# Kernel optimization log

Hardware: AMD Instinct MI355X
Metric: run time of the kernel (lower is better)

Reference implementation:

```python
import jax, jax.numpy as jnp
import numpy as np

THRESHOLD = 0.1
EPS = 1e-05


def setup_inputs() -> dict:
    key = jax.random.key(0)
    kx, kl, k1, k2 = jax.random.split(key, 4)
    B, S, D = 8, 4096, 1024
    Dh = max(2, D // 2)
    x = jax.random.normal(kx, (B, S, D), dtype=jnp.float32)
    # trailing (right) padding with random valid lengths in [S//2, S]
    lengths = jax.random.randint(kl, (B,), S // 2, S + 1)
    pad = jnp.arange(S)[None, :] >= lengths[:, None]  # [B, S] bool, True = padded
    W1 = jax.random.normal(k1, (D, Dh), dtype=jnp.float32) * (1.0 / np.sqrt(D))
    b1 = jnp.zeros((Dh,), dtype=jnp.float32)
    W2 = jax.random.normal(k2, (Dh, 1), dtype=jnp.float32) * (1.0 / np.sqrt(Dh))
    b2 = jnp.zeros((1,), dtype=jnp.float32)
    return {"x": x, "pad": pad, "W1": W1, "b1": b1, "W2": W2, "b2": b2}


def reference(x, pad, W1, b1, W2, b2):
    B, S, D = x.shape
    pos = jnp.arange(S)
    # number of valid (non-pad) tokens per batch; pad is trailing
    length = S - jnp.sum(pad, axis=1)  # [B]

    # tiny gate MLP: Linear -> ReLU -> Linear, squashed to (0, 1)
    h = jax.nn.relu(jnp.einsum('bsd,dh->bsh', x, W1) + b1)
    y = jnp.einsum('bsh,ho->bso', h, W2) + b2          # [B, S, 1]
    y = (1.0 + jnp.tanh(10.0 * y)) * 0.5

    # zero out gate values at padded positions (torch loop: y[i, n:] = 0)
    valid = pos[None, :] < length[:, None]             # [B, S]
    y = jnp.where(valid[..., None], y, 0.0)

    # lift so at least one token passes the threshold
    adjust = jnp.clip(EPS + THRESHOLD - jnp.max(y, axis=1), 0.0)  # [B, 1]
    y = y + adjust[:, None, :]                         # broadcast over seq

    u = x * y                                          # gated features [B, S, D]
    ys = y[..., 0]                                     # [B, S]
    u_mask = (ys > THRESHOLD) & (~pad)                 # tokens kept
    new_len = jnp.sum(u_mask, axis=1)                  # [B]

    # compact kept tokens to the front of each row (stable sort: kept first,
    # original order preserved) -- the mask-scatter v[v_mask] = u[u_mask]
    order = jnp.argsort(~u_mask, axis=1, stable=True)  # [B, S]
    v = jnp.take_along_axis(u, order[..., None], axis=1)
    v_mask = pos[None, :] < new_len[:, None]           # [B, S]
    v = jnp.where(v_mask[..., None], v, 0.0)
    v_pad = ~v_mask
    return v, v_pad
```

## Files before the change

### kernel.cpp

```cpp
#include <hip/hip_runtime.h>
#include <math.h>

#define NB 8
#define NS 4096
#define ND 1024
#define NDH 512
#define NTOK (NB*NS)
#define THRESH 0.1f
#define EPSV 1e-5f

using short8   = __attribute__((ext_vector_type(8)))  short;
using floatx16 = __attribute__((ext_vector_type(16))) float;
using floatv4  = __attribute__((ext_vector_type(4)))  float;

__device__ __forceinline__ unsigned short f32_to_bf16_rne(float f) {
  union { float f; unsigned u; } v; v.f = f;
  unsigned r = v.u + 0x7fffu + ((v.u >> 16) & 1u);
  return (unsigned short)(r >> 16);
}
__device__ __forceinline__ float bf16_to_f32(unsigned short h) {
  union { unsigned u; float f; } v; v.u = ((unsigned)h) << 16;
  return v.f;
}

__device__ __forceinline__ void cvt8_split(const float4& a, const float4& b,
                                           short8& hi, short8& lo) {
  float v8[8] = {a.x, a.y, a.z, a.w, b.x, b.y, b.z, b.w};
  unsigned hp[4], lp[4];
#pragma unroll
  for (int j = 0; j < 4; ++j) {
    unsigned short h0 = f32_to_bf16_rne(v8[2 * j]);
    unsigned short h1 = f32_to_bf16_rne(v8[2 * j + 1]);
    unsigned short l0 = f32_to_bf16_rne(v8[2 * j] - bf16_to_f32(h0));
    unsigned short l1 = f32_to_bf16_rne(v8[2 * j + 1] - bf16_to_f32(h1));
    hp[j] = (unsigned)h0 | ((unsigned)h1 << 16);
    lp[j] = (unsigned)l0 | ((unsigned)l1 << 16);
  }
  *(uint4*)&hi = make_uint4(hp[0], hp[1], hp[2], hp[3]);
  *(uint4*)&lo = make_uint4(lp[0], lp[1], lp[2], lp[3]);
}

__global__ __launch_bounds__(256)
void k0_prep(const float* __restrict__ W1, unsigned short* __restrict__ Wf,
             unsigned int* __restrict__ rowmax) {
  __shared__ float sw[16][513];
  const int t = threadIdx.x;
  const int k16 = blockIdx.x;
  if (k16 == 0 && t < NB) rowmax[t] = 0u;
#pragma unroll
  for (int i = 0; i < 8; ++i) {
    int flat = i * 256 + t;
    int r = flat >> 7, c4 = (flat & 127) << 2;
    *(float4*)&sw[r][c4] = *(const float4*)(W1 + (size_t)(k16 * 16 + r) * NDH + c4);
  }
  __syncthreads();
#pragma unroll
  for (int q = 0; q < 4; ++q) {
    int ss = q * 256 + t;
    int n32 = ss >> 6, lane = ss & 63;
    int n = n32 * 32 + (lane & 31);
    int kb = (lane >> 5) * 8;
    unsigned hi2[4], lo2[4];
#pragma unroll
    for (int j = 0; j < 4; ++j) {
      float w0 = sw[kb + 2 * j][n], w1 = sw[kb + 2 * j + 1][n];
      unsigned short h0 = f32_to_bf16_rne(w0), h1 = f32_to_bf16_rne(w1);
      unsigned short l0 = f32_to_bf16_rne(w0 - bf16_to_f32(h0));
      unsigned short l1 = f32_to_bf16_rne(w1 - bf16_to_f32(h1));
      hi2[j] = (unsigned)h0 | ((unsigned)h1 << 16);
      lo2[j] = (unsigned)l0 | ((unsigned)l1 << 16);
    }
    size_t cb = ((size_t)(n32 * 64 + k16) * 2) * 512 + (size_t)lane * 8;
    *(uint4*)(Wf + cb)       = make_uint4(hi2[0], hi2[1], hi2[2], hi2[3]);
    *(uint4*)(Wf + cb + 512) = make_uint4(lo2[0], lo2[1], lo2[2], lo2[3]);
  }
}

__global__ __launch_bounds__(256, 2)
void k1_gemm(const float* __restrict__ x, const unsigned short* __restrict__ Wf,
             const float* __restrict__ b1, const float* __restrict__ W2,
             const int* __restrict__ pad, const float* __restrict__ b2,
             float* __restrict__ ysq, unsigned int* __restrict__ rowmax) {
  __shared__ float red[4][64];

  const int tid = threadIdx.x;
  const int wave = tid >> 6, lane = tid & 63;
  const int l31 = lane & 31, h5 = lane >> 5;
  const int tok0 = blockIdx.x * 64;

  floatx16 acc[2][4];
#pragma unroll
  for (int mt = 0; mt < 2; ++mt)
#pragma unroll
    for (int nt = 0; nt < 4; ++nt)
#pragma unroll
      for (int r = 0; r < 16; ++r) acc[mt][nt][r] = 0.f;

  const float* xbase = x + (size_t)(tok0 + l31) * ND + h5 * 8;

  const unsigned short* wb[4];
#pragma unroll
  for (int nt = 0; nt < 4; ++nt)
    wb[nt] = Wf + (((size_t)(wave * 4 + nt) * 64) * 2) * 512 + (size_t)lane * 8;

  float4 xc[2][2][2], xn[2][2][2];
#pragma unroll
  for (int mt = 0; mt < 2; ++mt)
#pragma unroll
    for (int kh = 0; kh < 2; ++kh) {
      const float* xp = xbase + (size_t)mt * 32 * ND + kh * 16;
      xc[mt][kh][0] = *(const float4*)xp;
      xc[mt][kh][1] = *(const float4*)(xp + 4);
    }

  for (int it = 0; it < 32; ++it) {
    if (it < 31) {
#pragma unroll
      for (int mt = 0; mt < 2; ++mt)
#pragma unroll
        for (int kh = 0; kh < 2; ++kh) {
          const float* xp = xbase + (size_t)mt * 32 * ND + (it + 1) * 32 + kh * 16;
          xn[mt][kh][0] = *(const float4*)xp;
          xn[mt][kh][1] = *(const float4*)(xp + 4);
        }
    }
#pragma unroll
    for (int kh = 0; kh < 2; ++kh) {
      short8 bh[4], bl[4];
#pragma unroll
      for (int nt = 0; nt < 4; ++nt) {
        const unsigned short* q = wb[nt] + ((size_t)(2 * it + kh) * 2) * 512;
        bh[nt] = *(const short8*)(q);
        bl[nt] = *(const short8*)(q + 512);
      }
      short8 ah[2], al[2];
#pragma unroll
      for (int mt = 0; mt < 2; ++mt)
        cvt8_split(xc[mt][kh][0], xc[mt][kh][1], ah[mt], al[mt]);
#pragma unroll
      for (int nt = 0; nt < 4; ++nt)
#pragma unroll
        for (int mt = 0; mt < 2; ++mt)
          acc[mt][nt] = __builtin_amdgcn_mfma_f32_32x32x16_bf16(ah[mt], bh[nt], acc[mt][nt], 0, 0, 0);
#pragma unroll
      for (int nt = 0; nt < 4; ++nt)
#pragma unroll
        for (int mt = 0; mt < 2; ++mt)
          acc[mt][nt] = __builtin_amdgcn_mfma_f32_32x32x16_bf16(al[mt], bh[nt], acc[mt][nt], 0, 0, 0);
#pragma unroll
      for (int nt = 0; nt < 4; ++nt)
#pragma unroll
        for (int mt = 0; mt < 2; ++mt)
          acc[mt][nt] = __builtin_amdgcn_mfma_f32_32x32x16_bf16(ah[mt], bl[nt], acc[mt][nt], 0, 0, 0);
    }
    if (it < 31) {
#pragma unroll
      for (int mt = 0; mt < 2; ++mt)
#pragma unroll
        for (int kh = 0; kh < 2; ++kh) {
          xc[mt][kh][0] = xn[mt][kh][0];
          xc[mt][kh][1] = xn[mt][kh][1];
        }
    }
  }

  float b1v[4], w2v[4];
#pragma unroll
  for (int nt = 0; nt < 4; ++nt) {
    const int n = wave * 128 + nt * 32 + l31;
    b1v[nt] = b1[n];
    w2v[nt] = W2[n];
  }
#pragma unroll
  for (int mt = 0; mt < 2; ++mt) {
    float pr[16];
#pragma unroll
    for (int r = 0; r < 16; ++r) pr[r] = 0.f;
#pragma unroll
    for (int nt = 0; nt < 4; ++nt)
#pragma unroll
      for (int r = 0; r < 16; ++r)
        pr[r] += fmaxf(acc[mt][nt][r] + b1v[nt], 0.f) * w2v[nt];
#pragma unroll
    for (int m = 1; m <= 16; m <<= 1)
#pragma unroll
      for (int r = 0; r < 16; ++r) pr[r] += __shfl_xor(pr[r], m, 64);
    if (l31 == 0) {
#pragma unroll
      for (int r = 0; r < 16; ++r) {
        int row = (r & 3) + 8 * (r >> 2) + 4 * h5;
        red[wave][mt * 32 + row] = pr[r];
      }
    }
  }
  __syncthreads();
  if (tid < 64) {
    float s = red[0][tid] + red[1][tid] + red[2][tid] + red[3][tid];
    const int t = tok0 + tid;
    float yl = s + b2[0];
    float y = (1.f + tanhf(10.f * yl)) * 0.5f;
    if (pad[t]) y = 0.f;
    ysq[t] = y;
    float m = y;
#pragma unroll
    for (int o = 32; o >= 1; o >>= 1) m = fmaxf(m, __shfl_xor(m, o, 64));
    if (tid == 0) atomicMax(rowmax + (t >> 12), __float_as_uint(m));
  }
}

__global__ __launch_bounds__(256)
void k2b(const float* __restrict__ ysq, const int* __restrict__ pad,
         const unsigned int* __restrict__ rowmax, float* __restrict__ gval,
         int* __restrict__ src_of_dest, int* __restrict__ new_len,
         float* __restrict__ vpad_out) {
  __shared__ int ssum[4];
  const int b = blockIdx.x, tid = threadIdx.x;
  const int lane = tid & 63, wv = tid >> 6;
  const int base = b * NS, s0 = tid * 16;
  const float adj = fmaxf(EPSV + THRESH - __uint_as_float(rowmax[b]), 0.f);

  float yv[16];
  unsigned km = 0;
  int cnt = 0;
#pragma unroll
  for (int i = 0; i < 16; ++i) {
    int s = s0 + i;
    float yf = ysq[base + s] + adj;
    yv[i] = yf;
    bool keep = (yf > THRESH) && !pad[base + s];
    if (keep) { km |= (1u << i); ++cnt; }
  }
  int inc = cnt;
#pragma unroll
  for (int o = 1; o < 64; o <<= 1) {
    int tmp = __shfl_up(inc, o, 64);
    if (lane >= o) inc += tmp;
  }
  if (lane == 63) ssum[wv] = inc;
  __syncthreads();
  int wpre = 0;
  for (int w = 0; w < wv; ++w) wpre += ssum[w];
  const int total = ssum[0] + ssum[1] + ssum[2] + ssum[3];
  int off = wpre + inc - cnt;
#pragma unroll
  for (int i = 0; i < 16; ++i) {
    int s = s0 + i;
    if ((km >> i) & 1u) {
      src_of_dest[base + off] = s;
      gval[base + off] = yv[i];
      ++off;
    }
    vpad_out[base + s] = (s >= total) ? 1.f : 0.f;
  }
  if (tid == 0) new_len[b] = total;
}

__global__ __launch_bounds__(256)
void k3_gather(const float* __restrict__ x, const float* __restrict__ gval,
               const int* __restrict__ src_of_dest, const int* __restrict__ new_len,
               float* __restrict__ v) {
  const int slot0 = blockIdx.x * 16;
  const int b = slot0 >> 12;
  const int nl = new_len[b];
  const int tid = threadIdx.x;
#pragma unroll
  for (int i = 0; i < 16; ++i) {
    const int slot = slot0 + i;
    const int dest = slot & (NS - 1);
    floatv4* vo = (floatv4*)(v + (size_t)slot * ND);
    floatv4 r;
    if (dest < nl) {
      const int src = src_of_dest[slot];
      const float g = gval[slot];
      floatv4 xv = ((const floatv4*)(x + ((size_t)b * NS + src) * ND))[tid];
      r = xv * g;
    } else {
      r = (floatv4)(0.f);
    }
    __builtin_nontemporal_store(r, vo + tid);
  }
}

extern "C" void kernel_launch(void* const* d_in, const int* in_sizes, int n_in,
                              void* d_out, int out_size, void* d_ws, size_t ws_size,
                              hipStream_t stream) {
  const float* x   = (const float*)d_in[0];
  const int*   pad = (const int*)d_in[1];
  const float* W1  = (const float*)d_in[2];
  const float* b1  = (const float*)d_in[3];
  const float* W2  = (const float*)d_in[4];
  const float* b2  = (const float*)d_in[5];

  float* v    = (float*)d_out;
  float* vpad = v + (size_t)NTOK * ND;

  unsigned short* Wf = (unsigned short*)(v + 24000000);

  float* ysq  = (float*)d_ws;
  float* gval = ysq + NTOK;
  int* src    = (int*)(gval + NTOK);
  int* nlen   = src + NTOK;
  unsigned int* rowmax = (unsigned int*)(nlen + NB);

  k0_prep<<<64, 256, 0, stream>>>(W1, Wf, rowmax);
  k1_gemm<<<NTOK / 64, 256, 0, stream>>>(x, Wf, b1, W2, pad, b2, ysq, rowmax);
  k2b<<<NB, 256, 0, stream>>>(ysq, pad, rowmax, gval, src, nlen, vpad);
  k3_gather<<<NTOK / 16, 256, 0, stream>>>(x, gval, src, nlen, v);
}
```

Baseline: 335.7 us.

## Stage split-bf16 x tiles in LDS and widen compaction scan block

In the gate GEMM, each x element was previously converted to hi/lo bf16 by every wave in registers. Each thread now converts its slice of a 64x64 x tile once into double-buffered LDS, and the waves read their MFMA A fragments from that shared copy. This removes the 4x redundant global loads and conversions across waves, at the cost of LDS traffic and one barrier per K step. Separately, the per-row compaction kernel now uses 1024 threads with vectorized 4-element loads instead of 256 threads with 16 scalar loads each.

```diff
diff --git a/kernel.cpp b/kernel.cpp
--- a/kernel.cpp
+++ b/kernel.cpp
@@ -23,23 +23,6 @@
   return v.f;
 }
 
-__device__ __forceinline__ void cvt8_split(const float4& a, const float4& b,
-                                           short8& hi, short8& lo) {
-  float v8[8] = {a.x, a.y, a.z, a.w, b.x, b.y, b.z, b.w};
-  unsigned hp[4], lp[4];
-#pragma unroll
-  for (int j = 0; j < 4; ++j) {
-    unsigned short h0 = f32_to_bf16_rne(v8[2 * j]);
-    unsigned short h1 = f32_to_bf16_rne(v8[2 * j + 1]);
-    unsigned short l0 = f32_to_bf16_rne(v8[2 * j] - bf16_to_f32(h0));
-    unsigned short l1 = f32_to_bf16_rne(v8[2 * j + 1] - bf16_to_f32(h1));
-    hp[j] = (unsigned)h0 | ((unsigned)h1 << 16);
-    lp[j] = (unsigned)l0 | ((unsigned)l1 << 16);
-  }
-  *(uint4*)&hi = make_uint4(hp[0], hp[1], hp[2], hp[3]);
-  *(uint4*)&lo = make_uint4(lp[0], lp[1], lp[2], lp[3]);
-}
-
 __global__ __launch_bounds__(256)
 void k0_prep(const float* __restrict__ W1, unsigned short* __restrict__ Wf,
              unsigned int* __restrict__ rowmax) {
@@ -81,6 +64,7 @@
              const float* __restrict__ b1, const float* __restrict__ W2,
              const int* __restrict__ pad, const float* __restrict__ b2,
              float* __restrict__ ysq, unsigned int* __restrict__ rowmax) {
+  __shared__ __align__(16) unsigned short sx[2][2][64 * 72];
   __shared__ float red[4][64];
 
   const int tid = threadIdx.x;
@@ -96,47 +80,69 @@
 #pragma unroll
       for (int r = 0; r < 16; ++r) acc[mt][nt][r] = 0.f;
 
-  const float* xbase = x + (size_t)(tok0 + l31) * ND + h5 * 8;
+  const int sm = tid >> 2;
+  const int sk = (tid & 3) * 16;
+  const float* xrow = x + (size_t)(tok0 + sm) * ND + sk;
 
   const unsigned short* wb[4];
 #pragma unroll
   for (int nt = 0; nt < 4; ++nt)
     wb[nt] = Wf + (((size_t)(wave * 4 + nt) * 64) * 2) * 512 + (size_t)lane * 8;
 
-  float4 xc[2][2][2], xn[2][2][2];
-#pragma unroll
-  for (int mt = 0; mt < 2; ++mt)
-#pragma unroll
-    for (int kh = 0; kh < 2; ++kh) {
-      const float* xp = xbase + (size_t)mt * 32 * ND + kh * 16;
-      xc[mt][kh][0] = *(const float4*)xp;
-      xc[mt][kh][1] = *(const float4*)(xp + 4);
-    }
-
-  for (int it = 0; it < 32; ++it) {
-    if (it < 31) {
-#pragma unroll
-      for (int mt = 0; mt < 2; ++mt)
-#pragma unroll
-        for (int kh = 0; kh < 2; ++kh) {
-          const float* xp = xbase + (size_t)mt * 32 * ND + (it + 1) * 32 + kh * 16;
-          xn[mt][kh][0] = *(const float4*)xp;
-          xn[mt][kh][1] = *(const float4*)(xp + 4);
-        }
-    }
-#pragma unroll
-    for (int kh = 0; kh < 2; ++kh) {
+  auto stage_cvt = [&](int bf, const float4& a0, const float4& a1,
+                       const float4& a2, const float4& a3) {
+    float v16[16] = {a0.x, a0.y, a0.z, a0.w, a1.x, a1.y, a1.z, a1.w,
+                     a2.x, a2.y, a2.z, a2.w, a3.x, a3.y, a3.z, a3.w};
+    unsigned hp[8], lp[8];
+#pragma unroll
+    for (int j = 0; j < 8; ++j) {
+      unsigned short h0 = f32_to_bf16_rne(v16[2 * j]);
+      unsigned short h1 = f32_to_bf16_rne(v16[2 * j + 1]);
+      unsigned short l0 = f32_to_bf16_rne(v16[2 * j] - bf16_to_f32(h0));
+      unsigned short l1 = f32_to_bf16_rne(v16[2 * j + 1] - bf16_to_f32(h1));
+      hp[j] = (unsigned)h0 | ((unsigned)h1 << 16);
+      lp[j] = (unsigned)l0 | ((unsigned)l1 << 16);
+    }
+    *(uint4*)&sx[bf][0][sm * 72 + sk]     = make_uint4(hp[0], hp[1], hp[2], hp[3]);
+    *(uint4*)&sx[bf][0][sm * 72 + sk + 8] = make_uint4(hp[4], hp[5], hp[6], hp[7]);
+    *(uint4*)&sx[bf][1][sm * 72 + sk]     = make_uint4(lp[0], lp[1], lp[2], lp[3]);
+    *(uint4*)&sx[bf][1][sm * 72 + sk + 8] = make_uint4(lp[4], lp[5], lp[6], lp[7]);
+  };
+
+  {
+    float4 a0 = *(const float4*)xrow;
+    float4 a1 = *(const float4*)(xrow + 4);
+    float4 a2 = *(const float4*)(xrow + 8);
+    float4 a3 = *(const float4*)(xrow + 12);
+    stage_cvt(0, a0, a1, a2, a3);
+  }
+
+  for (int it = 0; it < 16; ++it) {
+    const int p = it & 1;
+    __syncthreads();
+    float4 pa0, pa1, pa2, pa3;
+    if (it < 15) {
+      const float* xp = xrow + (it + 1) * 64;
+      pa0 = *(const float4*)xp;
+      pa1 = *(const float4*)(xp + 4);
+      pa2 = *(const float4*)(xp + 8);
+      pa3 = *(const float4*)(xp + 12);
+    }
+#pragma unroll
+    for (int kh = 0; kh < 4; ++kh) {
       short8 bh[4], bl[4];
 #pragma unroll
       for (int nt = 0; nt < 4; ++nt) {
-        const unsigned short* q = wb[nt] + ((size_t)(2 * it + kh) * 2) * 512;
+        const unsigned short* q = wb[nt] + ((size_t)(4 * it + kh) * 2) * 512;
         bh[nt] = *(const short8*)(q);
         bl[nt] = *(const short8*)(q + 512);
       }
       short8 ah[2], al[2];
 #pragma unroll
-      for (int mt = 0; mt < 2; ++mt)
-        cvt8_split(xc[mt][kh][0], xc[mt][kh][1], ah[mt], al[mt]);
+      for (int mt = 0; mt < 2; ++mt) {
+        ah[mt] = *(const short8*)&sx[p][0][(mt * 32 + l31) * 72 + kh * 16 + h5 * 8];
+        al[mt] = *(const short8*)&sx[p][1][(mt * 32 + l31) * 72 + kh * 16 + h5 * 8];
+      }
 #pragma unroll
       for (int nt = 0; nt < 4; ++nt)
 #pragma unroll
@@ -153,15 +159,7 @@
         for (int mt = 0; mt < 2; ++mt)
           acc[mt][nt] = __builtin_amdgcn_mfma_f32_32x32x16_bf16(ah[mt], bl[nt], acc[mt][nt], 0, 0, 0);
     }
-    if (it < 31) {
-#pragma unroll
-      for (int mt = 0; mt < 2; ++mt)
-#pragma unroll
-        for (int kh = 0; kh < 2; ++kh) {
-          xc[mt][kh][0] = xn[mt][kh][0];
-          xc[mt][kh][1] = xn[mt][kh][1];
-        }
-    }
+    if (it < 15) stage_cvt(p ^ 1, pa0, pa1, pa2, pa3);
   }
 
   float b1v[4], w2v[4];
@@ -208,26 +206,26 @@
   }
 }
 
-__global__ __launch_bounds__(256)
+__global__ __launch_bounds__(1024)
 void k2b(const float* __restrict__ ysq, const int* __restrict__ pad,
          const unsigned int* __restrict__ rowmax, float* __restrict__ gval,
          int* __restrict__ src_of_dest, int* __restrict__ new_len,
          float* __restrict__ vpad_out) {
-  __shared__ int ssum[4];
+  __shared__ int ssum[16];
   const int b = blockIdx.x, tid = threadIdx.x;
   const int lane = tid & 63, wv = tid >> 6;
-  const int base = b * NS, s0 = tid * 16;
+  const int base = b * NS, s0 = tid * 4;
   const float adj = fmaxf(EPSV + THRESH - __uint_as_float(rowmax[b]), 0.f);
 
-  float yv[16];
+  float4 yq = *(const float4*)(ysq + base + s0);
+  int4 pq = *(const int4*)(pad + base + s0);
+  float yv[4] = {yq.x + adj, yq.y + adj, yq.z + adj, yq.w + adj};
+  int pv[4] = {pq.x, pq.y, pq.z, pq.w};
   unsigned km = 0;
   int cnt = 0;
 #pragma unroll
-  for (int i = 0; i < 16; ++i) {
-    int s = s0 + i;
-    float yf = ysq[base + s] + adj;
-    yv[i] = yf;
-    bool keep = (yf > THRESH) && !pad[base + s];
+  for (int i = 0; i < 4; ++i) {
+    bool keep = (yv[i] > THRESH) && !pv[i];
     if (keep) { km |= (1u << i); ++cnt; }
   }
   int inc = cnt;
@@ -239,11 +237,16 @@
   if (lane == 63) ssum[wv] = inc;
   __syncthreads();
   int wpre = 0;
-  for (int w = 0; w < wv; ++w) wpre += ssum[w];
-  const int total = ssum[0] + ssum[1] + ssum[2] + ssum[3];
+  int total = 0;
+#pragma unroll
+  for (int w = 0; w < 16; ++w) {
+    int sv = ssum[w];
+    if (w < wv) wpre += sv;
+    total += sv;
+  }
   int off = wpre + inc - cnt;
 #pragma unroll
-  for (int i = 0; i < 16; ++i) {
+  for (int i = 0; i < 4; ++i) {
     int s = s0 + i;
     if ((km >> i) & 1u) {
       src_of_dest[base + off] = s;
@@ -304,6 +307,6 @@
 
   k0_prep<<<64, 256, 0, stream>>>(W1, Wf, rowmax);
   k1_gemm<<<NTOK / 64, 256, 0, stream>>>(x, Wf, b1, W2, pad, b2, ysq, rowmax);
-  k2b<<<NB, 256, 0, stream>>>(ysq, pad, rowmax, gval, src, nlen, vpad);
+  k2b<<<NB, 1024, 0, stream>>>(ysq, pad, rowmax, gval, src, nlen, vpad);
   k3_gather<<<NTOK / 16, 256, 0, stream>>>(x, gval, src, nlen, v);
 }
```

Measured after the change: 315.4 us. 6.1% less time.
